# Kernel optimization log

Hardware: AMD Instinct MI355X
Metric: run time of the kernel (lower is better)

## Reference

```python
import jax, jax.numpy as jnp
import numpy as np
from jax import lax

B, T, D, H, W = 2, 8, 64, 64, 64
E, HID = 4, 256


def _layernorm(x, g, b, eps=1e-5):
    m = x.mean(-1, keepdims=True)
    v = ((x - m) ** 2).mean(-1, keepdims=True)
    return (x - m) / jnp.sqrt(v + eps) * g + b


def _pscan(A, X, axis):
    # linear recurrence h_t = A_t * h_{t-1} + X_t via associative scan
    def comb(l, r):
        a1, x1 = l
        a2, x2 = r
        return a2 * a1, a2 * x1 + x2
    return lax.associative_scan(comb, (A, X), axis=axis)[1]


def setup_inputs() -> dict:
    key = jax.random.key(0)
    ks = jax.random.split(key, 32)
    r = lambda i, shape, s=1.0: jax.random.normal(ks[i], shape, jnp.float32) * s
    D2 = 2 * D
    return {
        'x_re': r(0, (B, T, D, H, W)), 'x_im': r(1, (B, T, D, H, W)),
        'dt': jax.random.uniform(ks[2], (T,), jnp.float32, 0.5, 1.0),
        'ln_s_g': jnp.ones(D2), 'ln_s_b': jnp.zeros(D2),
        'conv_w': r(3, (3, 3, D2, D2), 0.03), 'conv_b': jnp.zeros(D2),
        'mom_w': r(4, (D2, D2), 0.08), 'mom_b': jnp.zeros(D2),
        'adv_w': jnp.full((1,), 0.1, jnp.float32),
        'enc_re': r(5, (D, D), 0.1), 'enc_im': r(6, (D, D), 0.1),
        'dec_re': r(7, (D, D), 0.1), 'dec_im': r(8, (D, D), 0.1),
        'flux_a_re': r(9, (D,)), 'flux_a_im': r(10, (D,), 0.1),
        'fin_re': r(11, (D, D), 0.1), 'fin_im': r(12, (D, D), 0.1),
        'fproj_re': r(13, (D, D), 0.1), 'fproj_im': r(14, (D, D), 0.1),
        'gate_w': r(15, (D2, D), 0.1), 'gate_b': jnp.zeros(D),
        'lam_re': r(16, (D,)), 'lam_im': r(17, (D,), 0.1),
        'noise_re': r(18, (B, T, H, W, D)), 'noise_im': r(19, (B, T, H, W, D)),
        'e_scale': jnp.full((1,), 0.1, jnp.float32),
        'ln_t_g': jnp.ones(D2), 'ln_t_b': jnp.zeros(D2),
        'router_w': r(20, (D2, E), 0.1), 'router_b': jnp.zeros(E),
        'w1': r(21, (E, D2, HID), 0.08), 'b1': jnp.zeros((E, HID)),
        'w2': r(22, (E, HID, D2), 0.08), 'b2': jnp.zeros((E, D2)),
    }


def _forward(x_re, x_im, dt, ln_s_g, ln_s_b, conv_w, conv_b, mom_w, mom_b, adv_w,
             enc_re, enc_im, dec_re, dec_im, flux_a_re, flux_a_im, fin_re, fin_im,
             fproj_re, fproj_im, gate_w, gate_b, lam_re, lam_im, noise_re, noise_im,
             e_scale, ln_t_g, ln_t_b, router_w, router_b, w1, b1, w2, b2):
    x = (x_re + 1j * x_im).astype(jnp.complex64)            # [B,T,D,H,W]
    target_energy = (jnp.abs(x) ** 2).mean(axis=(-2, -1))   # [B,T,D]
    momentum = x.mean(axis=(-2, -1))                        # [B,T,D] complex
    xcl = jnp.transpose(x, (0, 1, 3, 4, 2))                 # [B,T,H,W,D]
    Bs, Ts, Hs, Ws, Ds = xcl.shape
    D2 = 2 * Ds
    # --- spatial complex (Clifford) conv branch: LN over 2D channels + conv ---
    xr = jnp.concatenate([xcl.real, xcl.imag], -1)          # [B,T,H,W,2D]
    xn = _layernorm(xr, ln_s_g, ln_s_b)
    y = lax.conv_general_dilated(xn.reshape(Bs * Ts, Hs, Ws, D2), conv_w,
                                 (1, 1), 'SAME',
                                 dimension_numbers=('NHWC', 'HWIO', 'NHWC')) + conv_b
    y = y.reshape(Bs, Ts, Hs, Ws, D2)
    xcl = xcl + (y[..., :Ds] + 1j * y[..., Ds:])
    # --- momentum advection ---
    z_mean = xcl.mean(axis=(2, 3))                          # [B,T,D]
    mom_cat = jnp.concatenate([momentum.real, momentum.imag], -1) @ mom_w + mom_b
    mom_new = mom_cat[..., :Ds] + 1j * mom_cat[..., Ds:]
    dtb = jnp.broadcast_to(dt[None, :], (Bs, Ts))
    xcl = xcl + (mom_new * adv_w[0])[:, :, None, None, :] * dtb[:, :, None, None, None]
    momentum = 0.9 * momentum + 0.1 * z_mean
    # --- eigenbasis encode ---
    x_eigen = xcl @ (enc_re + 1j * enc_im)                  # [B,T,H,W,D]
    x_mean = x_eigen.mean(axis=(2, 3))                      # [B,T,D]
    # --- flux tracker: parallel scan over T ---
    A_flux = jnp.exp(-jax.nn.softplus(flux_a_re) + 1j * flux_a_im)
    A_flux = jnp.broadcast_to(A_flux, (Bs, Ts, Ds)).astype(jnp.complex64)
    X_flux = x_mean @ (fin_re + 1j * fin_im)
    flux_seq = _pscan(A_flux, X_flux, axis=1)               # [B,T,D]
    source = flux_seq @ (fproj_re + 1j * fproj_im)
    gate = jax.nn.sigmoid(jnp.concatenate([flux_seq.real, flux_seq.imag], -1) @ gate_w + gate_b)
    g = gate[:, :, None, None, :]
    forcing = x_eigen * g + source[:, :, None, None, :] * (1.0 - g)
    # --- temporal propagation: per-site parallel scan over T ---
    lam = -jax.nn.softplus(lam_re) + 1j * lam_im            # [D]
    op_decay = jnp.exp(lam[None, None, :] * dtb[:, :, None])  # [B,T,D]
    op_forcing = (op_decay - 1.0) / lam
    u_t = forcing * op_forcing[:, :, None, None, :]
    A_time = jnp.broadcast_to(op_decay[:, :, None, None, :], u_t.shape)
    u_out = _pscan(A_time, u_t, axis=1)                     # [B,T,H,W,D]
    noise = 0.01 * jnp.sqrt(dtb)[:, :, None, None, None] * (noise_re + 1j * noise_im)
    u_out = u_out + noise
    # --- decode + energy projection ---
    x_out = u_out @ (dec_re + 1j * dec_im)                  # [B,T,H,W,D]
    cur_e = (jnp.abs(x_out) ** 2).mean(axis=(2, 3))
    ratio = jnp.clip(target_energy / (cur_e + 1e-8), 0.5, 2.0)
    sf = jnp.sqrt(ratio)[:, :, None, None, :]
    x_out = x_out * (1.0 + e_scale[0] * (sf - 1.0))
    # --- temporal LN + MoE FFN on real-concat tokens ---
    xr2 = jnp.concatenate([x_out.real, x_out.imag], -1)
    xn2 = _layernorm(xr2, ln_t_g, ln_t_b)                   # [B,T,H,W,2D]
    tok = xn2.reshape(-1, D2)                               # [N,2D]
    p = jax.nn.softmax(tok @ router_w + router_b, -1)       # [N,E]
    hmid = jax.nn.gelu(jnp.einsum('nd,edh->neh', tok, w1) + b1)
    eout = jnp.einsum('neh,ehd->ned', hmid, w2) + b2
    out_tok = tok + jnp.einsum('ne,ned->nd', p, eout)
    out = out_tok.reshape(Bs, Ts, Hs, Ws, D2)
    x_out_c = out[..., :Ds] + 1j * out[..., Ds:]
    z_out = xcl + x_out_c
    z = jnp.transpose(z_out, (0, 1, 4, 2, 3))               # [B,T,D,H,W]
    return jnp.stack([z.real, z.imag])                      # [2,B,T,D,H,W]


def reference(x_re, x_im, dt, ln_s_g, ln_s_b, conv_w, conv_b, mom_w, mom_b, adv_w,
              enc_re, enc_im, dec_re, dec_im, flux_a_re, flux_a_im, fin_re, fin_im,
              fproj_re, fproj_im, gate_w, gate_b, lam_re, lam_im, noise_re, noise_im,
              e_scale, ln_t_g, ln_t_b, router_w, router_b, w1, b1, w2, b2):
    return _forward(x_re, x_im, dt, ln_s_g, ln_s_b, conv_w, conv_b, mom_w, mom_b, adv_w,
                    enc_re, enc_im, dec_re, dec_im, flux_a_re, flux_a_im, fin_re, fin_im,
                    fproj_re, fproj_im, gate_w, gate_b, lam_re, lam_im, noise_re, noise_im,
                    e_scale, ln_t_g, ln_t_b, router_w, router_b, w1, b1, w2, b2)
```

## Files before the change

### kernel.cpp

```cpp
#include <hip/hip_runtime.h>
#include <hip/hip_bf16.h>
#include <math.h>


#define W_XCL_RE 0u
#define W_XCL_IM 4194304u
#define W_C      8388608u
#define W_CWT    12582912u
#define W_W1T    14680064u
#define W_W2T    14745600u
#define W_ENCM   14811136u
#define W_DECM   14819328u
#define W_XMP_RE 14827520u
#define W_XMP_IM 14893056u
#define W_EP_RE  14958592u
#define W_EP_IM  15220736u
#define W_EIG_RE 16777216u
#define W_EIG_IM 20971520u
#define W_K1R    16777216u
#define W_K1I    16842752u
#define W_K1E    16908288u
#define W_SMALL  25165824u
#define W_TE     (W_SMALL+0u)
#define W_MOMRE  (W_SMALL+1024u)
#define W_MOMIM  (W_SMALL+2048u)
#define W_MTRE   (W_SMALL+3072u)
#define W_MTIM   (W_SMALL+4096u)
#define W_GATE   (W_SMALL+5120u)
#define W_SRCRE  (W_SMALL+6144u)
#define W_SRCIM  (W_SMALL+7168u)
#define W_OPFRE  (W_SMALL+8192u)
#define W_OPFIM  (W_SMALL+9216u)
#define W_OPDRE  (W_SMALL+10240u)
#define W_OPDIM  (W_SMALL+11264u)
#define W_SCALE  (W_SMALL+12288u)

typedef __attribute__((ext_vector_type(8))) short bf16x8;
typedef __attribute__((ext_vector_type(4))) float f32x4;

__device__ __forceinline__ unsigned short bfr(float x) {
  __hip_bfloat16 h = __float2bfloat16(x);
  return *(unsigned short*)&h;
}
__device__ __forceinline__ unsigned int pk2(float a, float b) {
  return ((unsigned int)bfr(b) << 16) | (unsigned int)bfr(a);
}

__global__ __launch_bounds__(256) void k2_transpose_ln(
    const float* __restrict__ xre, const float* __restrict__ xim,
    const float* __restrict__ g, const float* __restrict__ bb_, float* ws) {
  int blk = blockIdx.x; int bt = blk >> 6, h = blk & 63;
  __shared__ float tre[64][65], tim[64][65];
  __shared__ float ps[4][64], pq[4][64], pe[4][64];
  __shared__ float mean_l[64], rstd_l[64];
  size_t inbase = (size_t)bt * 262144 + (size_t)h * 64;
  for (int i = threadIdx.x; i < 1024; i += 256) {
    int d = i >> 4, w4 = (i & 15) * 4;
    float4 vr = *(const float4*)&xre[inbase + (size_t)d * 4096 + w4];
    float4 vi = *(const float4*)&xim[inbase + (size_t)d * 4096 + w4];
    tre[d][w4] = vr.x; tre[d][w4 + 1] = vr.y; tre[d][w4 + 2] = vr.z; tre[d][w4 + 3] = vr.w;
    tim[d][w4] = vi.x; tim[d][w4 + 1] = vi.y; tim[d][w4 + 2] = vi.z; tim[d][w4 + 3] = vi.w;
  }
  __syncthreads();
  {
    int w = threadIdx.x & 63, part = threadIdx.x >> 6;
    float s = 0.f, sq = 0.f;
    for (int dd = part * 16; dd < part * 16 + 16; dd++) {
      float vr = tre[dd][w], vi = tim[dd][w];
      s += vr + vi; sq += vr * vr + vi * vi;
    }
    ps[part][w] = s; pq[part][w] = sq;
  }
  __syncthreads();
  if (threadIdx.x < 64) {
    int w = threadIdx.x;
    float s  = ps[0][w] + ps[1][w] + ps[2][w] + ps[3][w];
    float sq = pq[0][w] + pq[1][w] + pq[2][w] + pq[3][w];
    float m = s / 128.f;
    float v = sq / 128.f - m * m;
    mean_l[w] = m; rstd_l[w] = rsqrtf(v + 1e-5f);
  }
  __syncthreads();
  {
    int d = threadIdx.x & 63, part = threadIdx.x >> 6;
    float sr = 0.f, si = 0.f, se = 0.f;
    for (int w = part * 16; w < part * 16 + 16; w++) {
      float vr = tre[d][w], vi = tim[d][w];
      sr += vr; si += vi; se += vr * vr + vi * vi;
    }
    ps[part][d] = sr; pq[part][d] = si; pe[part][d] = se;
  }
  __syncthreads();
  if (threadIdx.x < 64) {
    int d = threadIdx.x;
    int idx = h * 1024 + bt * 64 + d;
    ws[W_K1R + idx] = ps[0][d] + ps[1][d] + ps[2][d] + ps[3][d];
    ws[W_K1I + idx] = pq[0][d] + pq[1][d] + pq[2][d] + pq[3][d];
    ws[W_K1E + idx] = pe[0][d] + pe[1][d] + pe[2][d] + pe[3][d];
  }
  size_t tokbase = (size_t)blk * 64;
  for (int i = threadIdx.x; i < 1024; i += 256) {
    int w = i >> 4, d4 = (i & 15) * 4;
    float4 o, p;
    o.x = tre[d4][w]; o.y = tre[d4 + 1][w]; o.z = tre[d4 + 2][w]; o.w = tre[d4 + 3][w];
    p.x = tim[d4][w]; p.y = tim[d4 + 1][w]; p.z = tim[d4 + 2][w]; p.w = tim[d4 + 3][w];
    *(float4*)&ws[W_XCL_RE + tokbase * 64 + (size_t)w * 64 + d4] = o;
    *(float4*)&ws[W_XCL_IM + tokbase * 64 + (size_t)w * 64 + d4] = p;
  }
  __hip_bfloat16* xnb = (__hip_bfloat16*)(ws + W_C);
  int c0 = (threadIdx.x & 63) * 2, wg = threadIdx.x >> 6;
  float gc0 = g[c0], bc0 = bb_[c0], gc1 = g[c0 + 1], bc1 = bb_[c0 + 1];
  for (int pass = 0; pass < 16; pass++) {
    int w = pass * 4 + wg;
    float m = mean_l[w], rs = rstd_l[w];
    float v0 = (c0 < 64) ? tre[c0][w] : tim[c0 - 64][w];
    float v1 = (c0 + 1 < 64) ? tre[c0 + 1][w] : tim[c0 + 1 - 64][w];
    *(unsigned int*)&xnb[tokbase * 128 + (size_t)w * 128 + c0] =
        pk2((v0 - m) * rs * gc0 + bc0, (v1 - m) * rs * gc1 + bc1);
  }
}

__global__ void k1b_finish(float* ws) {
  int bt = blockIdx.x, d = threadIdx.x;
  float a = 0.f, b = 0.f, c = 0.f;
  for (int h = 0; h < 64; h++) {
    int idx = h * 1024 + bt * 64 + d;
    a += ws[W_K1R + idx]; b += ws[W_K1I + idx]; c += ws[W_K1E + idx];
  }
  ws[W_MOMRE + bt * 64 + d] = a / 4096.f;
  ws[W_MOMIM + bt * 64 + d] = b / 4096.f;
  ws[W_TE + bt * 64 + d]    = c / 4096.f;
}

__global__ void k2b_mom(const float* __restrict__ mom_w, const float* __restrict__ mom_b,
                        const float* __restrict__ adv_w, const float* __restrict__ dt, float* ws) {
  int bt = blockIdx.x; int t = bt & 7;
  __shared__ float mc[128], outl[128];
  int tid = threadIdx.x;
  mc[tid] = (tid < 64) ? ws[W_MOMRE + bt * 64 + tid] : ws[W_MOMIM + bt * 64 + tid - 64];
  __syncthreads();
  float acc = mom_b[tid];
  for (int k = 0; k < 128; k++) acc += mc[k] * mom_w[k * 128 + tid];
  outl[tid] = acc;
  __syncthreads();
  if (tid < 64) {
    float f = adv_w[0] * dt[t];
    ws[W_MTRE + bt * 64 + tid] = outl[tid] * f;
    ws[W_MTIM + bt * 64 + tid] = outl[64 + tid] * f;
  }
}

__global__ void k0_wprep(const float* __restrict__ w1, const float* __restrict__ w2,
                         const float* __restrict__ cw,
                         const float* __restrict__ enc_re, const float* __restrict__ enc_im,
                         const float* __restrict__ dec_re, const float* __restrict__ dec_im,
                         float* ws) {
  __hip_bfloat16* w1f = (__hip_bfloat16*)(ws + W_W1T);
  __hip_bfloat16* w2f = (__hip_bfloat16*)(ws + W_W2T);
  __hip_bfloat16* cwt = (__hip_bfloat16*)(ws + W_CWT);
  __hip_bfloat16* encM = (__hip_bfloat16*)(ws + W_ENCM);
  __hip_bfloat16* decM = (__hip_bfloat16*)(ws + W_DECM);
  int idx = blockIdx.x * 256 + threadIdx.x;
  if (idx < 131072) {
    {
      int j = idx & 7, lane = (idx >> 3) & 63, kt = (idx >> 9) & 3, nt = (idx >> 11) & 15, e = idx >> 15;
      int cout = nt * 16 + (lane & 15);
      int cin = kt * 32 + (lane >> 4) * 8 + j;
      w1f[idx] = __float2bfloat16(w1[((size_t)(e * 128 + cin)) * 256 + cout]);
    }
    {
      int j = idx & 7, lane = (idx >> 3) & 63, kt = (idx >> 9) & 7, nt = (idx >> 12) & 7, e = idx >> 15;
      int cout = nt * 16 + (lane & 15);
      int cin = kt * 32 + (lane >> 4) * 8 + j;
      w2f[idx] = __float2bfloat16(w2[((size_t)(e * 256 + cin)) * 128 + cout]);
    }
  }
  if (idx < 147456) {
    int j = idx & 7, lane = (idx >> 3) & 63, kt = (idx >> 9) & 3, r = idx >> 11;
    int nt = r & 7, tap = r >> 3;
    int cout = nt * 16 + (lane & 15);
    int cin = kt * 32 + (lane >> 4) * 8 + j;
    cwt[idx] = __float2bfloat16(cw[((size_t)(tap * 128 + cin)) * 128 + cout]);
  }
  if (idx < 16384) {
    int jj = idx & 7, lane = (idx >> 3) & 63, kt = (idx >> 9) & 3, nt = idx >> 11;
    int jc = nt * 16 + (lane & 15);
    int k = kt * 32 + (lane >> 4) * 8 + jj;
    float ve, vd;
    if (k < 64) {
      ve = (jc < 64) ? enc_re[k * 64 + jc] : enc_im[k * 64 + (jc - 64)];
      vd = (jc < 64) ? dec_re[k * 64 + jc] : dec_im[k * 64 + (jc - 64)];
    } else {
      int kk = k - 64;
      ve = (jc < 64) ? -enc_im[kk * 64 + jc] : enc_re[kk * 64 + (jc - 64)];
      vd = (jc < 64) ? -dec_im[kk * 64 + jc] : dec_re[kk * 64 + (jc - 64)];
    }
    encM[idx] = __float2bfloat16(ve);
    decM[idx] = __float2bfloat16(vd);
  }
}

__global__ __launch_bounds__(256) void k3_conv_enc(const float* __restrict__ cb, float* ws) {
  int blk = blockIdx.x; int bt = blk >> 6, h = blk & 63;
  const __hip_bfloat16* xnb = (const __hip_bfloat16*)(ws + W_C);
  const __hip_bfloat16* cwt = (const __hip_bfloat16*)(ws + W_CWT);
  const __hip_bfloat16* encM = (const __hip_bfloat16*)(ws + W_ENCM);
  __shared__ __align__(16) char smem[3 * 66 * 136 * 2];
  __hip_bfloat16 (*xin)[66][136] = (__hip_bfloat16(*)[66][136])smem;
  char* A = smem;
  int tid = threadIdx.x, lane = tid & 63, wv = tid >> 6;
  int arow = lane & 15, kgrp = (lane >> 4) * 8, rbase = (lane >> 4) * 4;

  for (int r = 0; r < 3; r++) {
    int hh = h + r - 1;
    if (hh < 0 || hh >= 64) {
      unsigned int* z = (unsigned int*)&xin[r][0][0];
      for (int i = tid; i < 4488; i += 256) z[i] = 0u;
    } else {
      if (tid < 68) *(unsigned int*)&xin[r][0][tid * 2] = 0u;
      else if (tid < 136) *(unsigned int*)&xin[r][65][(tid - 136 + 68) * 2] = 0u;
      const __hip_bfloat16* src = xnb + ((size_t)bt * 4096 + (size_t)hh * 64) * 128;
      for (int i = tid; i < 1024; i += 256) {
        int wp = (i >> 4) + 1, c8 = (i & 15) * 8;
        *(bf16x8*)&xin[r][wp][c8] = *(const bf16x8*)&src[(size_t)(wp - 1) * 128 + c8];
      }
    }
  }
  __syncthreads();

  f32x4 oacc[4][2];
  #pragma unroll
  for (int m = 0; m < 4; m++) {
    oacc[m][0] = (f32x4){0.f, 0.f, 0.f, 0.f};
    oacc[m][1] = (f32x4){0.f, 0.f, 0.f, 0.f};
  }

  for (int tap = 0; tap < 9; tap++) {
    int kh = tap / 3, kw = tap % 3;
    const __hip_bfloat16* wt0 = cwt + ((size_t)(tap * 8 + wv * 2) * 4) * 512 + lane * 8;
    #pragma unroll
    for (int kt = 0; kt < 4; kt++) {
      bf16x8 a[4];
      #pragma unroll
      for (int m = 0; m < 4; m++)
        a[m] = *(const bf16x8*)&xin[kh][m * 16 + arow + kw][kt * 32 + kgrp];
      bf16x8 b0 = *(const bf16x8*)&wt0[(size_t)kt * 512];
      bf16x8 b1 = *(const bf16x8*)&wt0[(size_t)(kt + 4) * 512];
      #pragma unroll
      for (int m = 0; m < 4; m++) {
        oacc[m][0] = __builtin_amdgcn_mfma_f32_16x16x32_bf16(a[m], b0, oacc[m][0], 0, 0, 0);
        oacc[m][1] = __builtin_amdgcn_mfma_f32_16x16x32_bf16(a[m], b1, oacc[m][1], 0, 0, 0);
      }
    }
  }
  __syncthreads();

  size_t rowtok = (size_t)blk * 64;
  #pragma unroll
  for (int n = 0; n < 2; n++) {
    int cout = (wv * 2 + n) * 16 + arow;
    bool isre = cout < 64;
    int d = cout & 63;
    float add = cb[cout] + ws[(isre ? W_MTRE : W_MTIM) + bt * 64 + d];
    float* xcl = ws + (isre ? W_XCL_RE : W_XCL_IM);
    #pragma unroll
    for (int m = 0; m < 4; m++)
      #pragma unroll
      for (int r = 0; r < 4; r++) {
        int w = m * 16 + rbase + r;
        float v = xcl[(rowtok + w) * 64 + d] + oacc[m][n][r] + add;
        xcl[(rowtok + w) * 64 + d] = v;
        *(__hip_bfloat16*)(A + w * 256 + ((cout * 2) ^ ((w & 7) << 4))) = __float2bfloat16(v);
      }
  }
  __syncthreads();

  f32x4 acc[4][2];
  #pragma unroll
  for (int m = 0; m < 4; m++) {
    acc[m][0] = (f32x4){0.f, 0.f, 0.f, 0.f};
    acc[m][1] = (f32x4){0.f, 0.f, 0.f, 0.f};
  }
  #pragma unroll
  for (int kt = 0; kt < 4; kt++) {
    bf16x8 a[4];
    #pragma unroll
    for (int m = 0; m < 4; m++)
      a[m] = *(const bf16x8*)(A + (m * 16 + arow) * 256 + (((kt * 32 + kgrp) * 2) ^ ((arow & 7) << 4)));
    bf16x8 b0 = *(const bf16x8*)&encM[(((size_t)(wv * 2 + 0) * 4 + kt) * 64 + lane) * 8];
    bf16x8 b1 = *(const bf16x8*)&encM[(((size_t)(wv * 2 + 1) * 4 + kt) * 64 + lane) * 8];
    #pragma unroll
    for (int m = 0; m < 4; m++) {
      acc[m][0] = __builtin_amdgcn_mfma_f32_16x16x32_bf16(a[m], b0, acc[m][0], 0, 0, 0);
      acc[m][1] = __builtin_amdgcn_mfma_f32_16x16x32_bf16(a[m], b1, acc[m][1], 0, 0, 0);
    }
  }
  float* orp = ws + W_EIG_RE;
  float* oip = ws + W_EIG_IM;
  #pragma unroll
  for (int n = 0; n < 2; n++) {
    int jc = (wv * 2 + n) * 16 + arow;
    float* dst = (jc < 64) ? orp : oip;
    int col = jc & 63;
    #pragma unroll
    for (int m = 0; m < 4; m++)
      #pragma unroll
      for (int r = 0; r < 4; r++)
        dst[(rowtok + m * 16 + rbase + r) * 64 + col] = acc[m][n][r];
    float s = 0.f;
    #pragma unroll
    for (int m = 0; m < 4; m++)
      #pragma unroll
      for (int r = 0; r < 4; r++) s += acc[m][n][r];
    s += __shfl_xor(s, 16);
    s += __shfl_xor(s, 32);
    if (lane < 16)
      ws[(jc < 64 ? W_XMP_RE : W_XMP_IM) + (size_t)blk * 64 + col] = s;
  }
}

__device__ __forceinline__ float softplusf(float x) {
  return (x > 20.f) ? x : log1pf(expf(x));
}

__global__ void k6_seq(const float* __restrict__ fin_re, const float* __restrict__ fin_im,
                       const float* __restrict__ fproj_re, const float* __restrict__ fproj_im,
                       const float* __restrict__ flux_a_re, const float* __restrict__ flux_a_im,
                       const float* __restrict__ gate_w, const float* __restrict__ gate_b,
                       const float* __restrict__ lam_re, const float* __restrict__ lam_im,
                       const float* __restrict__ dt, float* ws) {
  __shared__ float xmr[1024], xmi[1024], Xfr[1024], Xfi[1024], flr[1024], fli[1024];
  int tid = threadIdx.x;
  for (int i = tid; i < 1024; i += 256) {
    int bt = i >> 6, j = i & 63;
    float sr = 0.f, si = 0.f;
    for (int q = 0; q < 64; q++) {
      sr += ws[W_XMP_RE + (size_t)(bt * 64 + q) * 64 + j];
      si += ws[W_XMP_IM + (size_t)(bt * 64 + q) * 64 + j];
    }
    xmr[i] = sr / 4096.f; xmi[i] = si / 4096.f;
  }
  __syncthreads();
  for (int i = tid; i < 1024; i += 256) {
    int bt = i >> 6, j = i & 63;
    float ar = 0.f, ai = 0.f;
    for (int d = 0; d < 64; d++) {
      float xr = xmr[bt * 64 + d], xi = xmi[bt * 64 + d];
      float wr = fin_re[d * 64 + j], wi = fin_im[d * 64 + j];
      ar += xr * wr - xi * wi; ai += xr * wi + xi * wr;
    }
    Xfr[i] = ar; Xfi[i] = ai;
  }
  __syncthreads();
  if (tid < 128) {
    int b = tid >> 6, j = tid & 63;
    float mag = expf(-softplusf(flux_a_re[j]));
    float aar = mag * cosf(flux_a_im[j]), aai = mag * sinf(flux_a_im[j]);
    float sr = 0.f, si = 0.f;
    for (int t = 0; t < 8; t++) {
      int idx = (b * 8 + t) * 64 + j;
      float nr = aar * sr - aai * si + Xfr[idx];
      float ni = aar * si + aai * sr + Xfi[idx];
      sr = nr; si = ni;
      flr[idx] = sr; fli[idx] = si;
    }
  }
  __syncthreads();
  for (int i = tid; i < 1024; i += 256) {
    int bt = i >> 6, j = i & 63;
    float ar = 0.f, ai = 0.f, lg = 0.f;
    for (int d = 0; d < 64; d++) {
      float fr = flr[bt * 64 + d], fi = fli[bt * 64 + d];
      float wr = fproj_re[d * 64 + j], wi = fproj_im[d * 64 + j];
      ar += fr * wr - fi * wi; ai += fr * wi + fi * wr;
      lg += fr * gate_w[d * 64 + j] + fi * gate_w[(64 + d) * 64 + j];
    }
    ws[W_SRCRE + i] = ar; ws[W_SRCIM + i] = ai;
    ws[W_GATE + i] = 1.f / (1.f + expf(-(lg + gate_b[j])));
  }
  for (int i = tid; i < 1024; i += 256) {
    int bt = i >> 6, d = i & 63, t = bt & 7;
    float lr = -softplusf(lam_re[d]), li = lam_im[d];
    float dtv = dt[t];
    float mag = expf(lr * dtv);
    float dr = mag * cosf(li * dtv), di = mag * sinf(li * dtv);
    ws[W_OPDRE + i] = dr; ws[W_OPDIM + i] = di;
    float omr = dr - 1.f, omi = di;
    float den = lr * lr + li * li;
    ws[W_OPFRE + i] = (omr * lr + omi * li) / den;
    ws[W_OPFIM + i] = (omi * lr - omr * li) / den;
  }
}

__global__ __launch_bounds__(256) void k7_dec(const float* __restrict__ nre,
                                              const float* __restrict__ nim,
                                              const float* __restrict__ dt, float* ws) {
  int blk = blockIdx.x;
  int b = blk >> 8, h = (blk >> 2) & 63, wq = blk & 3;
  const __hip_bfloat16* decM = (const __hip_bfloat16*)(ws + W_DECM);
  __shared__ float gl[8][64], srl[8][64], sil[8][64], ofr[8][64], ofi[8][64], odr[8][64], odi[8][64];
  __shared__ __align__(16) char A[4096];
  __shared__ float dts[8];
  int tid = threadIdx.x, lane = tid & 63, wv = tid >> 6;
  int arow = lane & 15, kgrp = (lane >> 4) * 8, rbase = (lane >> 4) * 4;
  for (int i = tid; i < 512; i += 256) {
    int t = i >> 6, d = i & 63, idx = (b * 8 + t) * 64 + d;
    gl[t][d]  = ws[W_GATE + idx];
    srl[t][d] = ws[W_SRCRE + idx]; sil[t][d] = ws[W_SRCIM + idx];
    ofr[t][d] = ws[W_OPFRE + idx]; ofi[t][d] = ws[W_OPFIM + idx];
    odr[t][d] = ws[W_OPDRE + idx]; odi[t][d] = ws[W_OPDIM + idx];
  }
  if (tid < 8) dts[tid] = dt[tid];
  __syncthreads();

  int d = tid & 63, wbase = tid >> 6;
  float ur[4], ui[4];
  #pragma unroll
  for (int k = 0; k < 4; k++) { ur[k] = 0.f; ui[k] = 0.f; }

  for (int t = 0; t < 8; t++) {
    float ns = 0.01f * sqrtf(dts[t]);
    size_t tokb = ((size_t)(b * 8 + t) * 64 + h) * 64 + (size_t)wq * 16;
    #pragma unroll
    for (int k = 0; k < 4; k++) {
      int wl = wbase + 4 * k;
      size_t off = (tokb + wl) * 64 + d;
      float er_ = ws[W_EIG_RE + off], ei_ = ws[W_EIG_IM + off];
      float gg = gl[t][d];
      float fre = er_ * gg + srl[t][d] * (1.f - gg);
      float fim = ei_ * gg + sil[t][d] * (1.f - gg);
      float utr = fre * ofr[t][d] - fim * ofi[t][d];
      float uti = fre * ofi[t][d] + fim * ofr[t][d];
      float nur = odr[t][d] * ur[k] - odi[t][d] * ui[k] + utr;
      float nui = odr[t][d] * ui[k] + odi[t][d] * ur[k] + uti;
      ur[k] = nur; ui[k] = nui;
      float uor = nur + ns * nre[off];
      float uoi = nui + ns * nim[off];
      int sw = (wl & 7) << 4;
      *(__hip_bfloat16*)(A + wl * 256 + ((d * 2) ^ sw)) = __float2bfloat16(uor);
      *(__hip_bfloat16*)(A + wl * 256 + (((64 + d) * 2) ^ sw)) = __float2bfloat16(uoi);
    }
    __syncthreads();
    f32x4 acc[2];
    acc[0] = (f32x4){0.f, 0.f, 0.f, 0.f};
    acc[1] = (f32x4){0.f, 0.f, 0.f, 0.f};
    #pragma unroll
    for (int kt = 0; kt < 4; kt++) {
      bf16x8 a0 = *(const bf16x8*)(A + arow * 256 + (((kt * 32 + kgrp) * 2) ^ ((arow & 7) << 4)));
      bf16x8 b0 = *(const bf16x8*)&decM[(((size_t)(wv * 2 + 0) * 4 + kt) * 64 + lane) * 8];
      bf16x8 b1 = *(const bf16x8*)&decM[(((size_t)(wv * 2 + 1) * 4 + kt) * 64 + lane) * 8];
      acc[0] = __builtin_amdgcn_mfma_f32_16x16x32_bf16(a0, b0, acc[0], 0, 0, 0);
      acc[1] = __builtin_amdgcn_mfma_f32_16x16x32_bf16(a0, b1, acc[1], 0, 0, 0);
    }
    float* orp = ws + W_EIG_RE;
    float* oip = ws + W_EIG_IM;
    #pragma unroll
    for (int n = 0; n < 2; n++) {
      int jc = (wv * 2 + n) * 16 + arow;
      float* dst = (jc < 64) ? orp : oip;
      int col = jc & 63;
      #pragma unroll
      for (int r = 0; r < 4; r++)
        dst[(tokb + rbase + r) * 64 + col] = acc[n][r];
      float s = acc[n][0] * acc[n][0] + acc[n][1] * acc[n][1]
              + acc[n][2] * acc[n][2] + acc[n][3] * acc[n][3];
      s += __shfl_xor(s, 16);
      s += __shfl_xor(s, 32);
      if (lane < 16)
        ws[(jc < 64 ? W_EP_RE : W_EP_IM)
           + (size_t)((b * 8 + t) * 256 + h * 4 + wq) * 64 + col] = s;
    }
    __syncthreads();
  }
}

__global__ void k9b_scale(const float* __restrict__ escale, float* ws) {
  int bt = blockIdx.x; int j = threadIdx.x;
  float s = 0.f;
  for (int q = 0; q < 256; q++) {
    size_t idx = (size_t)(bt * 256 + q) * 64 + j;
    s += ws[W_EP_RE + idx] + ws[W_EP_IM + idx];
  }
  float cur = s / 4096.f;
  float te = ws[W_TE + bt * 64 + j];
  float ratio = te / (cur + 1e-8f);
  ratio = fminf(fmaxf(ratio, 0.5f), 2.0f);
  ws[W_SCALE + bt * 64 + j] = 1.f + escale[0] * (sqrtf(ratio) - 1.f);
}

__global__ __launch_bounds__(256) void k11_moe(
    const float* __restrict__ rw, const float* __restrict__ rb,
    const float* __restrict__ b1, const float* __restrict__ b2,
    const float* __restrict__ g2, const float* __restrict__ b2_,
    float* __restrict__ ws, float* __restrict__ out) {
  int blk = blockIdx.x; int bt = blk >> 6, h = blk & 63;
  const __hip_bfloat16* w1f = (const __hip_bfloat16*)(ws + W_W1T);
  const __hip_bfloat16* w2f = (const __hip_bfloat16*)(ws + W_W2T);
  __shared__ __align__(16) char bufA[33024];
  __shared__ __align__(16) char lt[16384];
  __shared__ float pl[64][4];
  __shared__ float sc[64];
  __shared__ float ps[4][64], pq[4][64], mean_l[64], rstd_l[64];
  char* hb = bufA;
  float (*obuf)[129] = (float(*)[129])bufA;
  int tid = threadIdx.x, lane = tid & 63, wv = tid >> 6;
  int arow = lane & 15, kgrp = (lane >> 4) * 8, rbase = (lane >> 4) * 4;
  size_t tokbase = (size_t)blk * 64;

  if (tid < 64) sc[tid] = ws[W_SCALE + bt * 64 + tid];
  __syncthreads();

  int w = tid >> 2, part = tid & 3;
  int c0 = part * 32, dbase = (part & 1) * 32;
  const float* rowp = ws + ((part < 2) ? W_EIG_RE : W_EIG_IM) + (tokbase + w) * 64 + dbase;
  float4 vv[8];
  {
    float s = 0.f, sq = 0.f;
    #pragma unroll
    for (int q = 0; q < 8; q++) {
      float4 t4 = *(const float4*)&rowp[q * 4];
      t4.x *= sc[dbase + q * 4 + 0];
      t4.y *= sc[dbase + q * 4 + 1];
      t4.z *= sc[dbase + q * 4 + 2];
      t4.w *= sc[dbase + q * 4 + 3];
      vv[q] = t4;
      s  += t4.x + t4.y + t4.z + t4.w;
      sq += t4.x * t4.x + t4.y * t4.y + t4.z * t4.z + t4.w * t4.w;
    }
    ps[part][w] = s; pq[part][w] = sq;
  }
  __syncthreads();
  if (tid < 64) {
    float s  = ps[0][tid] + ps[1][tid] + ps[2][tid] + ps[3][tid];
    float sq = pq[0][tid] + pq[1][tid] + pq[2][tid] + pq[3][tid];
    float m = s / 128.f, v = sq / 128.f - m * m;
    mean_l[tid] = m; rstd_l[tid] = rsqrtf(v + 1e-5f);
  }
  __syncthreads();
  {
    float m = mean_l[w], rs = rstd_l[w];
    int szw = (w & 7) << 4;
    #pragma unroll
    for (int q = 0; q < 8; q++) {
      int c = c0 + q * 4;
      float a0 = (vv[q].x - m) * rs * g2[c]     + b2_[c];
      float a1 = (vv[q].y - m) * rs * g2[c + 1] + b2_[c + 1];
      float a2 = (vv[q].z - m) * rs * g2[c + 2] + b2_[c + 2];
      float a3 = (vv[q].w - m) * rs * g2[c + 3] + b2_[c + 3];
      *(unsigned int*)(lt + w * 256 + ((c * 2) ^ szw)) = pk2(a0, a1);
      *(unsigned int*)(lt + w * 256 + (((c + 2) * 2) ^ szw)) = pk2(a2, a3);
    }
  }
  __syncthreads();
  {
    int l = tid >> 2, e = tid & 3;
    float acc = rb[e];
    const float* rwe = rw + e;
    int sz = (l & 7) << 4;
    for (int dd = 0; dd < 128; dd += 2) {
      unsigned int u = *(const unsigned int*)(lt + l * 256 + ((dd * 2) ^ sz));
      float x0 = __uint_as_float(u << 16);
      float x1 = __uint_as_float(u & 0xffff0000u);
      acc += x0 * rwe[dd * 4] + x1 * rwe[dd * 4 + 4];
    }
    pl[l][e] = acc;
  }
  __syncthreads();
  if (tid < 64) {
    float m = fmaxf(fmaxf(pl[tid][0], pl[tid][1]), fmaxf(pl[tid][2], pl[tid][3]));
    float e0 = expf(pl[tid][0] - m), e1 = expf(pl[tid][1] - m);
    float e2 = expf(pl[tid][2] - m), e3 = expf(pl[tid][3] - m);
    float s = e0 + e1 + e2 + e3;
    pl[tid][0] = e0 / s; pl[tid][1] = e1 / s; pl[tid][2] = e2 / s; pl[tid][3] = e3 / s;
  }

  f32x4 oacc[4][2];
  #pragma unroll
  for (int m = 0; m < 4; m++)
    #pragma unroll
    for (int n2 = 0; n2 < 2; n2++) {
      int col = (wv * 2 + n2) * 16 + arow;
      #pragma unroll
      for (int r = 0; r < 4; r++) {
        int row = m * 16 + rbase + r;
        oacc[m][n2][r] = __bfloat162float(
            *(const __hip_bfloat16*)(lt + row * 256 + ((col * 2) ^ ((row & 7) << 4))));
      }
    }
  __syncthreads();

  for (int e = 0; e < 4; e++) {
    #pragma unroll
    for (int hf = 0; hf < 2; hf++) {
      f32x4 acc1[4][2];
      #pragma unroll
      for (int m = 0; m < 4; m++) {
        acc1[m][0] = (f32x4){0.f, 0.f, 0.f, 0.f};
        acc1[m][1] = (f32x4){0.f, 0.f, 0.f, 0.f};
      }
      #pragma unroll
      for (int kt = 0; kt < 4; kt++) {
        bf16x8 a[4];
        #pragma unroll
        for (int m = 0; m < 4; m++) {
          int row = m * 16 + arow;
          a[m] = *(const bf16x8*)(lt + row * 256 + (((kt * 32 + kgrp) * 2) ^ ((arow & 7) << 4)));
        }
        bf16x8 b0 = *(const bf16x8*)&w1f[(((size_t)(e * 16 + wv * 4 + hf * 2 + 0) * 4 + kt) * 64 + lane) * 8];
        bf16x8 b1 = *(const bf16x8*)&w1f[(((size_t)(e * 16 + wv * 4 + hf * 2 + 1) * 4 + kt) * 64 + lane) * 8];
        #pragma unroll
        for (int m = 0; m < 4; m++) {
          acc1[m][0] = __builtin_amdgcn_mfma_f32_16x16x32_bf16(a[m], b0, acc1[m][0], 0, 0, 0);
          acc1[m][1] = __builtin_amdgcn_mfma_f32_16x16x32_bf16(a[m], b1, acc1[m][1], 0, 0, 0);
        }
      }
      if (hf == 0) __syncthreads();
      #pragma unroll
      for (int n = 0; n < 2; n++) {
        int col = (wv * 4 + hf * 2 + n) * 16 + arow;
        float bv = b1[e * 256 + col];
        #pragma unroll
        for (int m = 0; m < 4; m++)
          #pragma unroll
          for (int r = 0; r < 4; r++) {
            float hv = acc1[m][n][r] + bv;
            float z = 1.5957691216f * hv + 0.0713548162f * hv * hv * hv;
            float gelu = hv / (1.f + __expf(-z));
            int row = m * 16 + rbase + r;
            *(__hip_bfloat16*)(hb + row * 512 + ((col * 2) ^ ((row & 7) << 4))) =
                __float2bfloat16(gelu);
          }
      }
    }
    __syncthreads();
    f32x4 acc2[4][2];
    #pragma unroll
    for (int m = 0; m < 4; m++) {
      acc2[m][0] = (f32x4){0.f, 0.f, 0.f, 0.f};
      acc2[m][1] = (f32x4){0.f, 0.f, 0.f, 0.f};
    }
    #pragma unroll
    for (int kt = 0; kt < 8; kt++) {
      bf16x8 a2[4];
      #pragma unroll
      for (int m = 0; m < 4; m++) {
        int row = m * 16 + arow;
        a2[m] = *(const bf16x8*)(hb + row * 512 + (((kt * 32 + kgrp) * 2) ^ ((arow & 7) << 4)));
      }
      bf16x8 bb0 = *(const bf16x8*)&w2f[(((size_t)(e * 8 + wv * 2 + 0) * 8 + kt) * 64 + lane) * 8];
      bf16x8 bb1 = *(const bf16x8*)&w2f[(((size_t)(e * 8 + wv * 2 + 1) * 8 + kt) * 64 + lane) * 8];
      #pragma unroll
      for (int m = 0; m < 4; m++) {
        acc2[m][0] = __builtin_amdgcn_mfma_f32_16x16x32_bf16(a2[m], bb0, acc2[m][0], 0, 0, 0);
        acc2[m][1] = __builtin_amdgcn_mfma_f32_16x16x32_bf16(a2[m], bb1, acc2[m][1], 0, 0, 0);
      }
    }
    #pragma unroll
    for (int n = 0; n < 2; n++) {
      int col = (wv * 2 + n) * 16 + arow;
      float bv2 = b2[e * 128 + col];
      #pragma unroll
      for (int m = 0; m < 4; m++)
        #pragma unroll
        for (int r = 0; r < 4; r++)
          oacc[m][n][r] += pl[m * 16 + rbase + r][e] * (acc2[m][n][r] + bv2);
    }
  }

  __syncthreads();
  #pragma unroll
  for (int m = 0; m < 4; m++)
    #pragma unroll
    for (int n2 = 0; n2 < 2; n2++) {
      int col = (wv * 2 + n2) * 16 + arow;
      #pragma unroll
      for (int r = 0; r < 4; r++)
        obuf[m * 16 + rbase + r][col] = oacc[m][n2][r];
    }
  __syncthreads();

  {
    const float* xre = ws + W_XCL_RE;
    const float* xim = ws + W_XCL_IM;
    for (int i = tid; i < 8192; i += 256) {
      int wt = i >> 7, c = i & 127, dd = c & 63;
      float val = ((c < 64) ? xre : xim)[(tokbase + wt) * 64 + dd];
      obuf[wt][c] += val;
    }
  }
  __syncthreads();
  for (int i = tid; i < 8192; i += 256) {
    int d2 = i >> 6, wt = i & 63;
    out[(size_t)(d2 >> 6) * 4194304 + (size_t)bt * 262144 + (size_t)(d2 & 63) * 4096
        + (size_t)h * 64 + wt] = obuf[wt][d2];
  }
}

extern "C" void kernel_launch(void* const* d_in, const int* in_sizes, int n_in,
                              void* d_out, int out_size, void* d_ws, size_t ws_size,
                              hipStream_t stream) {
  const float* x_re      = (const float*)d_in[0];
  const float* x_im      = (const float*)d_in[1];
  const float* dt        = (const float*)d_in[2];
  const float* ln_s_g    = (const float*)d_in[3];
  const float* ln_s_b    = (const float*)d_in[4];
  const float* conv_w    = (const float*)d_in[5];
  const float* conv_b    = (const float*)d_in[6];
  const float* mom_w     = (const float*)d_in[7];
  const float* mom_b     = (const float*)d_in[8];
  const float* adv_w     = (const float*)d_in[9];
  const float* enc_re    = (const float*)d_in[10];
  const float* enc_im    = (const float*)d_in[11];
  const float* dec_re    = (const float*)d_in[12];
  const float* dec_im    = (const float*)d_in[13];
  const float* flux_a_re = (const float*)d_in[14];
  const float* flux_a_im = (const float*)d_in[15];
  const float* fin_re    = (const float*)d_in[16];
  const float* fin_im    = (const float*)d_in[17];
  const float* fproj_re  = (const float*)d_in[18];
  const float* fproj_im  = (const float*)d_in[19];
  const float* gate_w    = (const float*)d_in[20];
  const float* gate_b    = (const float*)d_in[21];
  const float* lam_re    = (const float*)d_in[22];
  const float* lam_im    = (const float*)d_in[23];
  const float* noise_re  = (const float*)d_in[24];
  const float* noise_im  = (const float*)d_in[25];
  const float* e_scale   = (const float*)d_in[26];
  const float* ln_t_g    = (const float*)d_in[27];
  const float* ln_t_b    = (const float*)d_in[28];
  const float* router_w  = (const float*)d_in[29];
  const float* router_b  = (const float*)d_in[30];
  const float* w1        = (const float*)d_in[31];
  const float* b1        = (const float*)d_in[32];
  const float* w2        = (const float*)d_in[33];
  const float* b2        = (const float*)d_in[34];
  float* ws  = (float*)d_ws;
  float* out = (float*)d_out;

  k0_wprep<<<576, 256, 0, stream>>>(w1, w2, conv_w, enc_re, enc_im, dec_re, dec_im, ws);
  k2_transpose_ln<<<1024, 256, 0, stream>>>(x_re, x_im, ln_s_g, ln_s_b, ws);
  k1b_finish<<<16, 64, 0, stream>>>(ws);
  k2b_mom<<<16, 128, 0, stream>>>(mom_w, mom_b, adv_w, dt, ws);
  k3_conv_enc<<<1024, 256, 0, stream>>>(conv_b, ws);
  k6_seq<<<1, 256, 0, stream>>>(fin_re, fin_im, fproj_re, fproj_im, flux_a_re, flux_a_im,
                                gate_w, gate_b, lam_re, lam_im, dt, ws);
  k7_dec<<<512, 256, 0, stream>>>(noise_re, noise_im, dt, ws);
  k9b_scale<<<16, 64, 0, stream>>>(e_scale, ws);
  k11_moe<<<1024, 256, 0, stream>>>(router_w, router_b, b1, b2, ln_t_g, ln_t_b, ws, out);
}
```

Baseline: 278.6 us.

## Split MoE hidden dim into halves to shrink shared memory and interleave GEMMs

The MoE kernel now computes the 256-wide hidden layer in two 128-column halves. Each half's GELU output feeds the second GEMM straight away, so the hidden staging buffer halves in size and the token tile and hidden buffer share one smaller shared allocation. Lower LDS use per block could allow more resident blocks per CU. The cost is an extra barrier per half, and divisions are replaced with hardware reciprocal approximations in the softmax and GELU, which slightly changes precision.

```diff
diff --git a/kernel.cpp b/kernel.cpp
--- a/kernel.cpp
+++ b/kernel.cpp
@@ -496,13 +496,13 @@
   int blk = blockIdx.x; int bt = blk >> 6, h = blk & 63;
   const __hip_bfloat16* w1f = (const __hip_bfloat16*)(ws + W_W1T);
   const __hip_bfloat16* w2f = (const __hip_bfloat16*)(ws + W_W2T);
-  __shared__ __align__(16) char bufA[33024];
-  __shared__ __align__(16) char lt[16384];
+  __shared__ __align__(16) char smem[33280];
   __shared__ float pl[64][4];
   __shared__ float sc[64];
   __shared__ float ps[4][64], pq[4][64], mean_l[64], rstd_l[64];
-  char* hb = bufA;
-  float (*obuf)[129] = (float(*)[129])bufA;
+  char* lt = smem;
+  char* hb = smem + 16384;
+  float (*obuf)[129] = (float(*)[129])smem;
   int tid = threadIdx.x, lane = tid & 63, wv = tid >> 6;
   int arow = lane & 15, kgrp = (lane >> 4) * 8, rbase = (lane >> 4) * 4;
   size_t tokbase = (size_t)blk * 64;
@@ -571,7 +571,8 @@
     float e0 = expf(pl[tid][0] - m), e1 = expf(pl[tid][1] - m);
     float e2 = expf(pl[tid][2] - m), e3 = expf(pl[tid][3] - m);
     float s = e0 + e1 + e2 + e3;
-    pl[tid][0] = e0 / s; pl[tid][1] = e1 / s; pl[tid][2] = e2 / s; pl[tid][3] = e3 / s;
+    float rs = __builtin_amdgcn_rcpf(s);
+    pl[tid][0] = e0 * rs; pl[tid][1] = e1 * rs; pl[tid][2] = e2 * rs; pl[tid][3] = e3 * rs;
   }
 
   f32x4 oacc[4][2];
@@ -590,8 +591,14 @@
   __syncthreads();
 
   for (int e = 0; e < 4; e++) {
-    #pragma unroll
-    for (int hf = 0; hf < 2; hf++) {
+    f32x4 acc2[4][2];
+    #pragma unroll
+    for (int m = 0; m < 4; m++) {
+      acc2[m][0] = (f32x4){0.f, 0.f, 0.f, 0.f};
+      acc2[m][1] = (f32x4){0.f, 0.f, 0.f, 0.f};
+    }
+    #pragma unroll
+    for (int hh = 0; hh < 2; hh++) {
       f32x4 acc1[4][2];
       #pragma unroll
       for (int m = 0; m < 4; m++) {
@@ -606,53 +613,48 @@
           int row = m * 16 + arow;
           a[m] = *(const bf16x8*)(lt + row * 256 + (((kt * 32 + kgrp) * 2) ^ ((arow & 7) << 4)));
         }
-        bf16x8 b0 = *(const bf16x8*)&w1f[(((size_t)(e * 16 + wv * 4 + hf * 2 + 0) * 4 + kt) * 64 + lane) * 8];
-        bf16x8 b1 = *(const bf16x8*)&w1f[(((size_t)(e * 16 + wv * 4 + hf * 2 + 1) * 4 + kt) * 64 + lane) * 8];
+        bf16x8 b0 = *(const bf16x8*)&w1f[(((size_t)(e * 16 + hh * 8 + wv * 2 + 0) * 4 + kt) * 64 + lane) * 8];
+        bf16x8 b1 = *(const bf16x8*)&w1f[(((size_t)(e * 16 + hh * 8 + wv * 2 + 1) * 4 + kt) * 64 + lane) * 8];
         #pragma unroll
         for (int m = 0; m < 4; m++) {
           acc1[m][0] = __builtin_amdgcn_mfma_f32_16x16x32_bf16(a[m], b0, acc1[m][0], 0, 0, 0);
           acc1[m][1] = __builtin_amdgcn_mfma_f32_16x16x32_bf16(a[m], b1, acc1[m][1], 0, 0, 0);
         }
       }
-      if (hf == 0) __syncthreads();
+      __syncthreads();
       #pragma unroll
       for (int n = 0; n < 2; n++) {
-        int col = (wv * 4 + hf * 2 + n) * 16 + arow;
-        float bv = b1[e * 256 + col];
+        int colh = (wv * 2 + n) * 16 + arow;
+        float bv = b1[e * 256 + hh * 128 + colh];
         #pragma unroll
         for (int m = 0; m < 4; m++)
           #pragma unroll
           for (int r = 0; r < 4; r++) {
             float hv = acc1[m][n][r] + bv;
             float z = 1.5957691216f * hv + 0.0713548162f * hv * hv * hv;
-            float gelu = hv / (1.f + __expf(-z));
+            float gelu = hv * __builtin_amdgcn_rcpf(1.f + __expf(-z));
             int row = m * 16 + rbase + r;
-            *(__hip_bfloat16*)(hb + row * 512 + ((col * 2) ^ ((row & 7) << 4))) =
+            *(__hip_bfloat16*)(hb + row * 256 + ((colh * 2) ^ ((row & 7) << 4))) =
                 __float2bfloat16(gelu);
           }
       }
-    }
-    __syncthreads();
-    f32x4 acc2[4][2];
-    #pragma unroll
-    for (int m = 0; m < 4; m++) {
-      acc2[m][0] = (f32x4){0.f, 0.f, 0.f, 0.f};
-      acc2[m][1] = (f32x4){0.f, 0.f, 0.f, 0.f};
-    }
-    #pragma unroll
-    for (int kt = 0; kt < 8; kt++) {
-      bf16x8 a2[4];
-      #pragma unroll
-      for (int m = 0; m < 4; m++) {
-        int row = m * 16 + arow;
-        a2[m] = *(const bf16x8*)(hb + row * 512 + (((kt * 32 + kgrp) * 2) ^ ((arow & 7) << 4)));
-      }
-      bf16x8 bb0 = *(const bf16x8*)&w2f[(((size_t)(e * 8 + wv * 2 + 0) * 8 + kt) * 64 + lane) * 8];
-      bf16x8 bb1 = *(const bf16x8*)&w2f[(((size_t)(e * 8 + wv * 2 + 1) * 8 + kt) * 64 + lane) * 8];
-      #pragma unroll
-      for (int m = 0; m < 4; m++) {
-        acc2[m][0] = __builtin_amdgcn_mfma_f32_16x16x32_bf16(a2[m], bb0, acc2[m][0], 0, 0, 0);
-        acc2[m][1] = __builtin_amdgcn_mfma_f32_16x16x32_bf16(a2[m], bb1, acc2[m][1], 0, 0, 0);
+      __syncthreads();
+      #pragma unroll
+      for (int kt2 = 0; kt2 < 4; kt2++) {
+        bf16x8 a2[4];
+        #pragma unroll
+        for (int m = 0; m < 4; m++) {
+          int row = m * 16 + arow;
+          a2[m] = *(const bf16x8*)(hb + row * 256 + (((kt2 * 32 + kgrp) * 2) ^ ((arow & 7) << 4)));
+        }
+        int ktg = hh * 4 + kt2;
+        bf16x8 bb0 = *(const bf16x8*)&w2f[(((size_t)(e * 8 + wv * 2 + 0) * 8 + ktg) * 64 + lane) * 8];
+        bf16x8 bb1 = *(const bf16x8*)&w2f[(((size_t)(e * 8 + wv * 2 + 1) * 8 + ktg) * 64 + lane) * 8];
+        #pragma unroll
+        for (int m = 0; m < 4; m++) {
+          acc2[m][0] = __builtin_amdgcn_mfma_f32_16x16x32_bf16(a2[m], bb0, acc2[m][0], 0, 0, 0);
+          acc2[m][1] = __builtin_amdgcn_mfma_f32_16x16x32_bf16(a2[m], bb1, acc2[m][1], 0, 0, 0);
+        }
       }
     }
     #pragma unroll
```

After: 296.8 us. 1.07x slower.
